# Performance work log

Hardware: AMD Instinct MI355X
Metric: run time of the kernel (lower is better)

Reference implementation:

```python
import jax, jax.numpy as jnp
import numpy as np

N = 65536          # total nodes (64 graphs x 1024 nodes)
E = 1048576        # total edges (avg degree 16)
F_IN, F_HID, F_OUT = 128, 128, 64


def setup_inputs() -> dict:
    key = jax.random.key(0)
    k1, k2, k3, k4, k5, k6, k7, k8 = jax.random.split(key, 8)
    x = jax.random.normal(k1, (N, F_IN), dtype=jnp.float32)
    edge_index = jax.random.randint(k2, (2, E), 0, N, dtype=jnp.int32)
    edge_weight = jax.random.uniform(k3, (E,), dtype=jnp.float32)
    batch = jnp.repeat(jnp.arange(64, dtype=jnp.int32), N // 64)
    s1 = 1.0 / np.sqrt(F_IN)
    s2 = 1.0 / np.sqrt(F_HID)
    W1 = jax.random.uniform(k4, (F_IN, F_HID), jnp.float32, -s1, s1)
    b1 = jnp.zeros((F_HID,), jnp.float32)
    W2 = jax.random.uniform(k5, (F_HID, F_HID), jnp.float32, -s2, s2)
    b2 = jnp.zeros((F_HID,), jnp.float32)
    fcW = jax.random.uniform(k6, (F_HID, F_OUT), jnp.float32, -s2, s2)
    fcb = jax.random.uniform(k7, (F_OUT,), jnp.float32, -s2, s2)
    return {"x": x, "edge_index": edge_index, "edge_weight": edge_weight,
            "batch": batch, "W1": W1, "b1": b1, "W2": W2, "b2": b2,
            "fcW": fcW, "fcb": fcb}


def gcn_conv(x, W, b, src, dst, ew, n_nodes):
    # PyG GCNConv: add self-loops (weight 1), symmetric normalization
    # deg[i] = 1 + sum of incoming edge weights at i
    deg = jax.ops.segment_sum(ew, dst, num_segments=n_nodes) + 1.0
    dinv = jax.lax.rsqrt(deg)                       # deg >= 1, no inf
    h = x @ W                                       # [N, F_out]
    norm = dinv[src] * ew * dinv[dst]               # [E]
    agg = jax.ops.segment_sum(h[src] * norm[:, None], dst, num_segments=n_nodes)
    agg = agg + h * (dinv * dinv)[:, None]          # self-loop term (1/deg)
    return agg + b


def reference(x, edge_index, edge_weight, batch, W1, b1, W2, b2, fcW, fcb):
    src, dst = edge_index[0], edge_index[1]
    n = x.shape[0]
    h = jax.nn.relu(gcn_conv(x, W1, b1, src, dst, edge_weight, n))
    h = jax.nn.relu(gcn_conv(h, W2, b2, src, dst, edge_weight, n))
    out = h @ fcW + fcb
    batch_size = int(batch.max()) + 1
    num_nodes = n // batch_size
    return out.reshape(batch_size, num_nodes, -1)
```

## Files before the change

### kernel.cpp

```cpp
#include <hip/hip_runtime.h>
#include <hip/hip_fp16.h>

#define N_NODES 65536
#define N_EDGES 1048576
#define F 128
#define NBUCK 256
#define BCAP 8192

typedef unsigned long long ull;
typedef _Float16 half8 __attribute__((ext_vector_type(8)));
typedef float floatx4 __attribute__((ext_vector_type(4)));


__global__ __launch_bounds__(256) void k_bpart(const int* __restrict__ srcArr,
                                               const int* __restrict__ dstArr,
                                               const float* __restrict__ ew,
                                               int* __restrict__ gfill,
                                               ull* __restrict__ brec) {
    __shared__ int hist[NBUCK];
    __shared__ int cur[NBUCK];
    int t = threadIdx.x;
    hist[t] = 0;
    __syncthreads();
    int base = blockIdx.x * 4096;
    int dv[16];
#pragma unroll
    for (int i = 0; i < 16; ++i) {
        dv[i] = dstArr[base + i * 256 + t];
        atomicAdd(&hist[dv[i] >> 8], 1);
    }
    __syncthreads();
    cur[t] = t * BCAP + atomicAdd(&gfill[t], hist[t]);
    __syncthreads();
#pragma unroll
    for (int i = 0; i < 16; ++i) {
        int e = base + i * 256 + t;
        int d = dv[i];
        unsigned int s = (unsigned int)srcArr[e];
        unsigned int wb = __float_as_uint(ew[e]);
        int pos = atomicAdd(&cur[d >> 8], 1);
        brec[pos] = ((ull)wb << 32) | ((ull)(d & 255) << 16) | (ull)s;
    }
}


__global__ __launch_bounds__(256) void k_build(const ull* __restrict__ brec,
                                               const int* __restrict__ gfill,
                                               float* __restrict__ dinv,
                                               ull* __restrict__ row_info,
                                               ull* __restrict__ edge8) {
    __shared__ ull packed[256];
    __shared__ int sc[256];
    __shared__ int cur[256];
    int t = threadIdx.x;
    int b = blockIdx.x;
    int cnt = gfill[b];
    int beg0 = b * BCAP;
    packed[t] = 0ULL;
    __syncthreads();

    for (int j = t; j < cnt; j += 256) {
        ull r = brec[beg0 + j];
        int dloc = (int)((r >> 16) & 255);
        float w = __uint_as_float((unsigned int)(r >> 32));
        ull fx = (ull)(w * 1073741824.0f);
        atomicAdd(&packed[dloc], (1ULL << 40) | fx);
    }
    __syncthreads();

    ull p = packed[t];
    int c = (int)(p >> 40);
    float deg = 1.0f + (float)(p & ((1ULL << 40) - 1)) * (1.0f / 1073741824.0f);
    dinv[b * 256 + t] = rsqrtf(deg);

    sc[t] = c;
    __syncthreads();
    for (int off = 1; off < 256; off <<= 1) {
        int tv = (t >= off) ? sc[t - off] : 0;
        __syncthreads();
        sc[t] += tv;
        __syncthreads();
    }
    int excl = sc[t] - c;
    row_info[b * 256 + t] = ((ull)(beg0 + excl) << 16) | (ull)c;
    cur[t] = beg0 + excl;
    __syncthreads();

    for (int j = t; j < cnt; j += 256) {
        ull r = brec[beg0 + j];
        int dloc = (int)((r >> 16) & 255);
        int pos = atomicAdd(&cur[dloc], 1);
        edge8[pos] = (r & 0xFFFFFFFF00000000ULL) | (r & 0xFFFFULL);
    }
}


__global__ __launch_bounds__(256) void k_gemm_mfma(const float* __restrict__ X,
                                                   const float* __restrict__ W,
                                                   const float* __restrict__ dinv,
                                                   __half* __restrict__ Y) {
    __shared__ _Float16 Ah[128][40];
    __shared__ _Float16 Al[128][40];
    __shared__ _Float16 Bh[128][40];
    __shared__ _Float16 Bl[128][40];

    const int tid = threadIdx.x;
    const int wv = tid >> 6;
    const int ln = tid & 63;
    const long rowbase = (long)blockIdx.x * 128;

    floatx4 acc[2][8];
#pragma unroll
    for (int i = 0; i < 2; ++i)
#pragma unroll
        for (int j = 0; j < 8; ++j) acc[i][j] = (floatx4)(0.f);

    for (int k0 = 0; k0 < 128; k0 += 32) {
        {
            int row = tid >> 1;
            int kh = (tid & 1) * 16;
            const float* src = &X[(rowbase + row) * 128 + k0 + kh];
            _Float16 hi[16], lo[16];
#pragma unroll
            for (int i = 0; i < 16; i += 4) {
                float4 v = *(const float4*)&src[i];
                hi[i + 0] = (_Float16)v.x; lo[i + 0] = (_Float16)(v.x - (float)hi[i + 0]);
                hi[i + 1] = (_Float16)v.y; lo[i + 1] = (_Float16)(v.y - (float)hi[i + 1]);
                hi[i + 2] = (_Float16)v.z; lo[i + 2] = (_Float16)(v.z - (float)hi[i + 2]);
                hi[i + 3] = (_Float16)v.w; lo[i + 3] = (_Float16)(v.w - (float)hi[i + 3]);
            }
            *(half8*)&Ah[row][kh] = *(half8*)&hi[0];
            *(half8*)&Ah[row][kh + 8] = *(half8*)&hi[8];
            *(half8*)&Al[row][kh] = *(half8*)&lo[0];
            *(half8*)&Al[row][kh + 8] = *(half8*)&lo[8];
        }
        {
            int n = tid & 127;
            int kh = (tid >> 7) * 16;
            _Float16 hi[16], lo[16];
#pragma unroll
            for (int i = 0; i < 16; ++i) {
                float v = W[(k0 + kh + i) * 128 + n];
                hi[i] = (_Float16)v;
                lo[i] = (_Float16)(v - (float)hi[i]);
            }
            *(half8*)&Bh[n][kh] = *(half8*)&hi[0];
            *(half8*)&Bh[n][kh + 8] = *(half8*)&hi[8];
            *(half8*)&Bl[n][kh] = *(half8*)&lo[0];
            *(half8*)&Bl[n][kh + 8] = *(half8*)&lo[8];
        }
        __syncthreads();

        int arow0 = wv * 32 + (ln & 15);
        int kq = (ln >> 4) * 8;
        half8 a_hi0 = *(const half8*)&Ah[arow0][kq];
        half8 a_hi1 = *(const half8*)&Ah[arow0 + 16][kq];
        half8 a_lo0 = *(const half8*)&Al[arow0][kq];
        half8 a_lo1 = *(const half8*)&Al[arow0 + 16][kq];
#pragma unroll
        for (int ct = 0; ct < 8; ++ct) {
            int bcol = ct * 16 + (ln & 15);
            half8 b_hi = *(const half8*)&Bh[bcol][kq];
            half8 b_lo = *(const half8*)&Bl[bcol][kq];
            acc[0][ct] = __builtin_amdgcn_mfma_f32_16x16x32_f16(a_hi0, b_hi, acc[0][ct], 0, 0, 0);
            acc[0][ct] = __builtin_amdgcn_mfma_f32_16x16x32_f16(a_hi0, b_lo, acc[0][ct], 0, 0, 0);
            acc[0][ct] = __builtin_amdgcn_mfma_f32_16x16x32_f16(a_lo0, b_hi, acc[0][ct], 0, 0, 0);
            acc[1][ct] = __builtin_amdgcn_mfma_f32_16x16x32_f16(a_hi1, b_hi, acc[1][ct], 0, 0, 0);
            acc[1][ct] = __builtin_amdgcn_mfma_f32_16x16x32_f16(a_hi1, b_lo, acc[1][ct], 0, 0, 0);
            acc[1][ct] = __builtin_amdgcn_mfma_f32_16x16x32_f16(a_lo1, b_hi, acc[1][ct], 0, 0, 0);
        }
        __syncthreads();
    }

#pragma unroll
    for (int rt = 0; rt < 2; ++rt)
#pragma unroll
        for (int reg = 0; reg < 4; ++reg) {
            long row = rowbase + wv * 32 + rt * 16 + (ln >> 4) * 4 + reg;
            float dv = dinv[row];
#pragma unroll
            for (int ct = 0; ct < 8; ++ct)
                Y[row * 128 + ct * 16 + (ln & 15)] = __float2half(acc[rt][ct][reg] * dv);
        }
}


__global__ __launch_bounds__(256) void k_gemm_mfma_h(const __half* __restrict__ X,
                                                     const float* __restrict__ W,
                                                     const float* __restrict__ dinv,
                                                     __half* __restrict__ Y) {
    __shared__ _Float16 Ah[128][40];
    __shared__ _Float16 Bh[128][40];
    __shared__ _Float16 Bl[128][40];

    const int tid = threadIdx.x;
    const int wv = tid >> 6;
    const int ln = tid & 63;
    const long rowbase = (long)blockIdx.x * 128;

    floatx4 acc[2][8];
#pragma unroll
    for (int i = 0; i < 2; ++i)
#pragma unroll
        for (int j = 0; j < 8; ++j) acc[i][j] = (floatx4)(0.f);

    for (int k0 = 0; k0 < 128; k0 += 32) {
        {
            int row = tid >> 1;
            int kh = (tid & 1) * 16;
            const __half* src = &X[(rowbase + row) * 128 + k0 + kh];
            *(half8*)&Ah[row][kh] = *(const half8*)&src[0];
            *(half8*)&Ah[row][kh + 8] = *(const half8*)&src[8];
        }
        {
            int n = tid & 127;
            int kh = (tid >> 7) * 16;
            _Float16 hi[16], lo[16];
#pragma unroll
            for (int i = 0; i < 16; ++i) {
                float v = W[(k0 + kh + i) * 128 + n];
                hi[i] = (_Float16)v;
                lo[i] = (_Float16)(v - (float)hi[i]);
            }
            *(half8*)&Bh[n][kh] = *(half8*)&hi[0];
            *(half8*)&Bh[n][kh + 8] = *(half8*)&hi[8];
            *(half8*)&Bl[n][kh] = *(half8*)&lo[0];
            *(half8*)&Bl[n][kh + 8] = *(half8*)&lo[8];
        }
        __syncthreads();

        int arow0 = wv * 32 + (ln & 15);
        int kq = (ln >> 4) * 8;
        half8 a0 = *(const half8*)&Ah[arow0][kq];
        half8 a1 = *(const half8*)&Ah[arow0 + 16][kq];
#pragma unroll
        for (int ct = 0; ct < 8; ++ct) {
            int bcol = ct * 16 + (ln & 15);
            half8 b_hi = *(const half8*)&Bh[bcol][kq];
            half8 b_lo = *(const half8*)&Bl[bcol][kq];
            acc[0][ct] = __builtin_amdgcn_mfma_f32_16x16x32_f16(a0, b_hi, acc[0][ct], 0, 0, 0);
            acc[0][ct] = __builtin_amdgcn_mfma_f32_16x16x32_f16(a0, b_lo, acc[0][ct], 0, 0, 0);
            acc[1][ct] = __builtin_amdgcn_mfma_f32_16x16x32_f16(a1, b_hi, acc[1][ct], 0, 0, 0);
            acc[1][ct] = __builtin_amdgcn_mfma_f32_16x16x32_f16(a1, b_lo, acc[1][ct], 0, 0, 0);
        }
        __syncthreads();
    }

#pragma unroll
    for (int rt = 0; rt < 2; ++rt)
#pragma unroll
        for (int reg = 0; reg < 4; ++reg) {
            long row = rowbase + wv * 32 + rt * 16 + (ln >> 4) * 4 + reg;
            float dv = dinv[row];
#pragma unroll
            for (int ct = 0; ct < 8; ++ct)
                Y[row * 128 + ct * 16 + (ln & 15)] = __float2half(acc[rt][ct][reg] * dv);
        }
}


__global__ __launch_bounds__(256) void k_fc_mfma_h(const __half* __restrict__ X,
                                                   const float* __restrict__ W,
                                                   const float* __restrict__ bias,
                                                   float* __restrict__ Y) {
    __shared__ _Float16 Ah[128][40];
    __shared__ _Float16 Bh[64][40];
    __shared__ _Float16 Bl[64][40];

    const int tid = threadIdx.x;
    const int wv = tid >> 6;
    const int ln = tid & 63;
    const long rowbase = (long)blockIdx.x * 128;

    floatx4 acc[2][4];
#pragma unroll
    for (int i = 0; i < 2; ++i)
#pragma unroll
        for (int j = 0; j < 4; ++j) acc[i][j] = (floatx4)(0.f);

    for (int k0 = 0; k0 < 128; k0 += 32) {
        {
            int row = tid >> 1;
            int kh = (tid & 1) * 16;
            const __half* src = &X[(rowbase + row) * 128 + k0 + kh];
            *(half8*)&Ah[row][kh] = *(const half8*)&src[0];
            *(half8*)&Ah[row][kh + 8] = *(const half8*)&src[8];
        }
        {
            int n = tid & 63;
            int kh = (tid >> 6) * 8;
            _Float16 hi[8], lo[8];
#pragma unroll
            for (int i = 0; i < 8; ++i) {
                float v = W[(k0 + kh + i) * 64 + n];
                hi[i] = (_Float16)v;
                lo[i] = (_Float16)(v - (float)hi[i]);
            }
            *(half8*)&Bh[n][kh] = *(half8*)&hi[0];
            *(half8*)&Bl[n][kh] = *(half8*)&lo[0];
        }
        __syncthreads();

        int arow0 = wv * 32 + (ln & 15);
        int kq = (ln >> 4) * 8;
        half8 a0 = *(const half8*)&Ah[arow0][kq];
        half8 a1 = *(const half8*)&Ah[arow0 + 16][kq];
#pragma unroll
        for (int ct = 0; ct < 4; ++ct) {
            int bcol = ct * 16 + (ln & 15);
            half8 b_hi = *(const half8*)&Bh[bcol][kq];
            half8 b_lo = *(const half8*)&Bl[bcol][kq];
            acc[0][ct] = __builtin_amdgcn_mfma_f32_16x16x32_f16(a0, b_hi, acc[0][ct], 0, 0, 0);
            acc[0][ct] = __builtin_amdgcn_mfma_f32_16x16x32_f16(a0, b_lo, acc[0][ct], 0, 0, 0);
            acc[1][ct] = __builtin_amdgcn_mfma_f32_16x16x32_f16(a1, b_hi, acc[1][ct], 0, 0, 0);
            acc[1][ct] = __builtin_amdgcn_mfma_f32_16x16x32_f16(a1, b_lo, acc[1][ct], 0, 0, 0);
        }
        __syncthreads();
    }

#pragma unroll
    for (int rt = 0; rt < 2; ++rt)
#pragma unroll
        for (int ct = 0; ct < 4; ++ct)
#pragma unroll
            for (int reg = 0; reg < 4; ++reg) {
                long row = rowbase + wv * 32 + rt * 16 + (ln >> 4) * 4 + reg;
                int col = ct * 16 + (ln & 15);
                Y[row * 64 + col] = acc[rt][ct][reg] + bias[col];
            }
}


__global__ __launch_bounds__(256) void k_aggregate(const __half2* __restrict__ hlin,
                                                   const ull* __restrict__ row_info,
                                                   const ull* __restrict__ edge8,
                                                   const float* __restrict__ dinv,
                                                   const float* __restrict__ bias,
                                                   __half2* __restrict__ out) {
    int wave = threadIdx.x >> 6;
    int lane = threadIdx.x & 63;
    int n = (blockIdx.x << 2) + wave;

    float di = dinv[n];
    ull info = row_info[n];
    int beg = (int)(info >> 16);
    int end = beg + (int)(info & 0xFFFF);

    float2 h0 = __half22float2(hlin[(size_t)n * 64 + lane]);
    float2 a0, a1, a2, a3, a4, a5, a6, a7;
    a0 = a1 = a2 = a3 = a4 = a5 = a6 = a7 = make_float2(0.f, 0.f);

    for (int jb = beg; jb < end; jb += 64) {
        int nload = end - jb;
        if (nload > 64) nload = 64;
        ull r = 0ULL;
        if (lane < nload) r = __builtin_nontemporal_load(&edge8[jb + lane]);
        for (int q = 0; q < nload; q += 8) {
            ull r0 = __shfl(r, q + 0), r1 = __shfl(r, q + 1);
            ull r2 = __shfl(r, q + 2), r3 = __shfl(r, q + 3);
            ull r4 = __shfl(r, q + 4), r5 = __shfl(r, q + 5);
            ull r6 = __shfl(r, q + 6), r7 = __shfl(r, q + 7);
            int s0 = (int)(r0 & 0xFFFF), s1 = (int)(r1 & 0xFFFF);
            int s2 = (int)(r2 & 0xFFFF), s3 = (int)(r3 & 0xFFFF);
            int s4 = (int)(r4 & 0xFFFF), s5 = (int)(r5 & 0xFFFF);
            int s6 = (int)(r6 & 0xFFFF), s7 = (int)(r7 & 0xFFFF);
            float c0 = __uint_as_float((unsigned int)(r0 >> 32));
            float c1 = __uint_as_float((unsigned int)(r1 >> 32));
            float c2 = __uint_as_float((unsigned int)(r2 >> 32));
            float c3 = __uint_as_float((unsigned int)(r3 >> 32));
            float c4 = __uint_as_float((unsigned int)(r4 >> 32));
            float c5 = __uint_as_float((unsigned int)(r5 >> 32));
            float c6 = __uint_as_float((unsigned int)(r6 >> 32));
            float c7 = __uint_as_float((unsigned int)(r7 >> 32));
            __half2 g0 = hlin[(size_t)s0 * 64 + lane];
            __half2 g1 = hlin[(size_t)s1 * 64 + lane];
            __half2 g2 = hlin[(size_t)s2 * 64 + lane];
            __half2 g3 = hlin[(size_t)s3 * 64 + lane];
            __half2 g4 = hlin[(size_t)s4 * 64 + lane];
            __half2 g5 = hlin[(size_t)s5 * 64 + lane];
            __half2 g6 = hlin[(size_t)s6 * 64 + lane];
            __half2 g7 = hlin[(size_t)s7 * 64 + lane];
            float2 f0 = __half22float2(g0), f1 = __half22float2(g1);
            float2 f2 = __half22float2(g2), f3 = __half22float2(g3);
            float2 f4 = __half22float2(g4), f5 = __half22float2(g5);
            float2 f6 = __half22float2(g6), f7 = __half22float2(g7);
            a0.x = fmaf(c0, f0.x, a0.x); a0.y = fmaf(c0, f0.y, a0.y);
            a1.x = fmaf(c1, f1.x, a1.x); a1.y = fmaf(c1, f1.y, a1.y);
            a2.x = fmaf(c2, f2.x, a2.x); a2.y = fmaf(c2, f2.y, a2.y);
            a3.x = fmaf(c3, f3.x, a3.x); a3.y = fmaf(c3, f3.y, a3.y);
            a4.x = fmaf(c4, f4.x, a4.x); a4.y = fmaf(c4, f4.y, a4.y);
            a5.x = fmaf(c5, f5.x, a5.x); a5.y = fmaf(c5, f5.y, a5.y);
            a6.x = fmaf(c6, f6.x, a6.x); a6.y = fmaf(c6, f6.y, a6.y);
            a7.x = fmaf(c7, f7.x, a7.x); a7.y = fmaf(c7, f7.y, a7.y);
        }
    }

    float2 sum;
    sum.x = ((a0.x + a1.x) + (a2.x + a3.x)) + ((a4.x + a5.x) + (a6.x + a7.x));
    sum.y = ((a0.y + a1.y) + (a2.y + a3.y)) + ((a4.y + a5.y) + (a6.y + a7.y));

    float2 bb = ((const float2*)bias)[lane];
    float ox = fmaxf(fmaf(di, sum.x + h0.x, bb.x), 0.f);
    float oy = fmaxf(fmaf(di, sum.y + h0.y, bb.y), 0.f);
    out[(size_t)n * 64 + lane] = __floats2half2_rn(ox, oy);
}


extern "C" void kernel_launch(void* const* d_in, const int* in_sizes, int n_in,
                              void* d_out, int out_size, void* d_ws, size_t ws_size,
                              hipStream_t stream) {
    const float* x   = (const float*)d_in[0];
    const int*   ei  = (const int*)d_in[1];
    const float* ew  = (const float*)d_in[2];
    const float* W1  = (const float*)d_in[4];
    const float* b1  = (const float*)d_in[5];
    const float* W2  = (const float*)d_in[6];
    const float* b2  = (const float*)d_in[7];
    const float* fcW = (const float*)d_in[8];
    const float* fcb = (const float*)d_in[9];
    float* out = (float*)d_out;

    const int* srcArr = ei;
    const int* dstArr = ei + N_EDGES;

    char* w = (char*)d_ws;
    int* gfill = (int*)w;              w += 256 * 4;
    float* dinv = (float*)w;           w += (size_t)N_NODES * 4;
    ull* row_info = (ull*)w;           w += (size_t)N_NODES * 8;
    ull* edge8 = (ull*)w;              w += (size_t)NBUCK * BCAP * 8;
    __half* bufH = (__half*)w;         w += (size_t)N_NODES * F * 2;
    __half* bufB = (__half*)w;         w += (size_t)N_NODES * F * 2;
    ull* brec = (ull*)bufH;

    hipMemsetAsync(gfill, 0, 256 * 4, stream);
    k_bpart<<<N_EDGES / 4096, 256, 0, stream>>>(srcArr, dstArr, ew, gfill, brec);
    k_build<<<NBUCK, 256, 0, stream>>>(brec, gfill, dinv, row_info, edge8);

    k_gemm_mfma<<<512, 256, 0, stream>>>(x, W1, dinv, bufH);
    k_aggregate<<<N_NODES / 4, 256, 0, stream>>>((const __half2*)bufH, row_info, edge8,
                                                 dinv, b1, (__half2*)bufB);
    k_gemm_mfma_h<<<512, 256, 0, stream>>>(bufB, W2, dinv, bufH);
    k_aggregate<<<N_NODES / 4, 256, 0, stream>>>((const __half2*)bufH, row_info, edge8,
                                                 dinv, b2, (__half2*)bufB);
    k_fc_mfma_h<<<512, 256, 0, stream>>>(bufB, fcW, fcb, out);
}
```

Measured before the change: 153.8 us.

## Fuse second-layer aggregation with final FC projection and replace memset with kernel

The second aggregation kernel now also does the final linear layer. Each block stages the full 128x64 fp32 fcW matrix in shared memory, each wave writes its node's ReLU activations to LDS, and the wave then computes the 64 outputs with scalar FMAs. This removes the separate MFMA FC kernel and the fp16 intermediate round trip through global memory. In exchange, every one of the 16384 blocks reloads 32 KB of weights and holds about 34 KB of LDS, which may cut occupancy for the latency-bound gather. The hipMemsetAsync on the bucket counters is also replaced by a tiny zeroing kernel.

```diff
diff --git a/kernel.cpp b/kernel.cpp
--- a/kernel.cpp
+++ b/kernel.cpp
@@ -10,6 +10,11 @@
 typedef unsigned long long ull;
 typedef _Float16 half8 __attribute__((ext_vector_type(8)));
 typedef float floatx4 __attribute__((ext_vector_type(4)));
+
+
+__global__ __launch_bounds__(256) void k_zero256(int* gfill) {
+    gfill[threadIdx.x] = 0;
+}
 
 
 __global__ __launch_bounds__(256) void k_bpart(const int* __restrict__ srcArr,
@@ -256,78 +261,6 @@
             for (int ct = 0; ct < 8; ++ct)
                 Y[row * 128 + ct * 16 + (ln & 15)] = __float2half(acc[rt][ct][reg] * dv);
         }
-}
-
-
-__global__ __launch_bounds__(256) void k_fc_mfma_h(const __half* __restrict__ X,
-                                                   const float* __restrict__ W,
-                                                   const float* __restrict__ bias,
-                                                   float* __restrict__ Y) {
-    __shared__ _Float16 Ah[128][40];
-    __shared__ _Float16 Bh[64][40];
-    __shared__ _Float16 Bl[64][40];
-
-    const int tid = threadIdx.x;
-    const int wv = tid >> 6;
-    const int ln = tid & 63;
-    const long rowbase = (long)blockIdx.x * 128;
-
-    floatx4 acc[2][4];
-#pragma unroll
-    for (int i = 0; i < 2; ++i)
-#pragma unroll
-        for (int j = 0; j < 4; ++j) acc[i][j] = (floatx4)(0.f);
-
-    for (int k0 = 0; k0 < 128; k0 += 32) {
-        {
-            int row = tid >> 1;
-            int kh = (tid & 1) * 16;
-            const __half* src = &X[(rowbase + row) * 128 + k0 + kh];
-            *(half8*)&Ah[row][kh] = *(const half8*)&src[0];
-            *(half8*)&Ah[row][kh + 8] = *(const half8*)&src[8];
-        }
-        {
-            int n = tid & 63;
-            int kh = (tid >> 6) * 8;
-            _Float16 hi[8], lo[8];
-#pragma unroll
-            for (int i = 0; i < 8; ++i) {
-                float v = W[(k0 + kh + i) * 64 + n];
-                hi[i] = (_Float16)v;
-                lo[i] = (_Float16)(v - (float)hi[i]);
-            }
-            *(half8*)&Bh[n][kh] = *(half8*)&hi[0];
-            *(half8*)&Bl[n][kh] = *(half8*)&lo[0];
-        }
-        __syncthreads();
-
-        int arow0 = wv * 32 + (ln & 15);
-        int kq = (ln >> 4) * 8;
-        half8 a0 = *(const half8*)&Ah[arow0][kq];
-        half8 a1 = *(const half8*)&Ah[arow0 + 16][kq];
-#pragma unroll
-        for (int ct = 0; ct < 4; ++ct) {
-            int bcol = ct * 16 + (ln & 15);
-            half8 b_hi = *(const half8*)&Bh[bcol][kq];
-            half8 b_lo = *(const half8*)&Bl[bcol][kq];
-            acc[0][ct] = __builtin_amdgcn_mfma_f32_16x16x32_f16(a0, b_hi, acc[0][ct], 0, 0, 0);
-            acc[0][ct] = __builtin_amdgcn_mfma_f32_16x16x32_f16(a0, b_lo, acc[0][ct], 0, 0, 0);
-            acc[1][ct] = __builtin_amdgcn_mfma_f32_16x16x32_f16(a1, b_hi, acc[1][ct], 0, 0, 0);
-            acc[1][ct] = __builtin_amdgcn_mfma_f32_16x16x32_f16(a1, b_lo, acc[1][ct], 0, 0, 0);
-        }
-        __syncthreads();
-    }
-
-#pragma unroll
-    for (int rt = 0; rt < 2; ++rt)
-#pragma unroll
-        for (int ct = 0; ct < 4; ++ct)
-#pragma unroll
-            for (int reg = 0; reg < 4; ++reg) {
-                long row = rowbase + wv * 32 + rt * 16 + (ln >> 4) * 4 + reg;
-                int col = ct * 16 + (ln & 15);
-                Y[row * 64 + col] = acc[rt][ct][reg] + bias[col];
-            }
 }
 
 
@@ -406,6 +339,104 @@
 }
 
 
+__global__ __launch_bounds__(256) void k_aggregate_fc(const __half2* __restrict__ hlin,
+                                                      const ull* __restrict__ row_info,
+                                                      const ull* __restrict__ edge8,
+                                                      const float* __restrict__ dinv,
+                                                      const float* __restrict__ bias,
+                                                      const float* __restrict__ fcW,
+                                                      const float* __restrict__ fcb,
+                                                      float* __restrict__ outF) {
+    __shared__ float Ws[128 * 64];
+    __shared__ float acts[4][128];
+
+    int tid = threadIdx.x;
+    int wave = tid >> 6;
+    int lane = tid & 63;
+    int n = (blockIdx.x << 2) + wave;
+
+    {
+        const float4* src = (const float4*)fcW;
+        float4* dst = (float4*)Ws;
+        for (int i = tid; i < 2048; i += 256) dst[i] = src[i];
+    }
+    __syncthreads();
+
+    float di = dinv[n];
+    ull info = row_info[n];
+    int beg = (int)(info >> 16);
+    int end = beg + (int)(info & 0xFFFF);
+
+    float2 h0 = __half22float2(hlin[(size_t)n * 64 + lane]);
+    float2 a0, a1, a2, a3, a4, a5, a6, a7;
+    a0 = a1 = a2 = a3 = a4 = a5 = a6 = a7 = make_float2(0.f, 0.f);
+
+    for (int jb = beg; jb < end; jb += 64) {
+        int nload = end - jb;
+        if (nload > 64) nload = 64;
+        ull r = 0ULL;
+        if (lane < nload) r = __builtin_nontemporal_load(&edge8[jb + lane]);
+        for (int q = 0; q < nload; q += 8) {
+            ull r0 = __shfl(r, q + 0), r1 = __shfl(r, q + 1);
+            ull r2 = __shfl(r, q + 2), r3 = __shfl(r, q + 3);
+            ull r4 = __shfl(r, q + 4), r5 = __shfl(r, q + 5);
+            ull r6 = __shfl(r, q + 6), r7 = __shfl(r, q + 7);
+            int s0 = (int)(r0 & 0xFFFF), s1 = (int)(r1 & 0xFFFF);
+            int s2 = (int)(r2 & 0xFFFF), s3 = (int)(r3 & 0xFFFF);
+            int s4 = (int)(r4 & 0xFFFF), s5 = (int)(r5 & 0xFFFF);
+            int s6 = (int)(r6 & 0xFFFF), s7 = (int)(r7 & 0xFFFF);
+            float c0 = __uint_as_float((unsigned int)(r0 >> 32));
+            float c1 = __uint_as_float((unsigned int)(r1 >> 32));
+            float c2 = __uint_as_float((unsigned int)(r2 >> 32));
+            float c3 = __uint_as_float((unsigned int)(r3 >> 32));
+            float c4 = __uint_as_float((unsigned int)(r4 >> 32));
+            float c5 = __uint_as_float((unsigned int)(r5 >> 32));
+            float c6 = __uint_as_float((unsigned int)(r6 >> 32));
+            float c7 = __uint_as_float((unsigned int)(r7 >> 32));
+            __half2 g0 = hlin[(size_t)s0 * 64 + lane];
+            __half2 g1 = hlin[(size_t)s1 * 64 + lane];
+            __half2 g2 = hlin[(size_t)s2 * 64 + lane];
+            __half2 g3 = hlin[(size_t)s3 * 64 + lane];
+            __half2 g4 = hlin[(size_t)s4 * 64 + lane];
+            __half2 g5 = hlin[(size_t)s5 * 64 + lane];
+            __half2 g6 = hlin[(size_t)s6 * 64 + lane];
+            __half2 g7 = hlin[(size_t)s7 * 64 + lane];
+            float2 f0 = __half22float2(g0), f1 = __half22float2(g1);
+            float2 f2 = __half22float2(g2), f3 = __half22float2(g3);
+            float2 f4 = __half22float2(g4), f5 = __half22float2(g5);
+            float2 f6 = __half22float2(g6), f7 = __half22float2(g7);
+            a0.x = fmaf(c0, f0.x, a0.x); a0.y = fmaf(c0, f0.y, a0.y);
+            a1.x = fmaf(c1, f1.x, a1.x); a1.y = fmaf(c1, f1.y, a1.y);
+            a2.x = fmaf(c2, f2.x, a2.x); a2.y = fmaf(c2, f2.y, a2.y);
+            a3.x = fmaf(c3, f3.x, a3.x); a3.y = fmaf(c3, f3.y, a3.y);
+            a4.x = fmaf(c4, f4.x, a4.x); a4.y = fmaf(c4, f4.y, a4.y);
+            a5.x = fmaf(c5, f5.x, a5.x); a5.y = fmaf(c5, f5.y, a5.y);
+            a6.x = fmaf(c6, f6.x, a6.x); a6.y = fmaf(c6, f6.y, a6.y);
+            a7.x = fmaf(c7, f7.x, a7.x); a7.y = fmaf(c7, f7.y, a7.y);
+        }
+    }
+
+    float2 sum;
+    sum.x = ((a0.x + a1.x) + (a2.x + a3.x)) + ((a4.x + a5.x) + (a6.x + a7.x));
+    sum.y = ((a0.y + a1.y) + (a2.y + a3.y)) + ((a4.y + a5.y) + (a6.y + a7.y));
+
+    float2 bb = ((const float2*)bias)[lane];
+    float ox = fmaxf(fmaf(di, sum.x + h0.x, bb.x), 0.f);
+    float oy = fmaxf(fmaf(di, sum.y + h0.y, bb.y), 0.f);
+
+    acts[wave][lane * 2]     = ox;
+    acts[wave][lane * 2 + 1] = oy;
+    __builtin_amdgcn_wave_barrier();
+
+    float o = fcb[lane];
+    const float* arow = acts[wave];
+#pragma unroll 8
+    for (int k = 0; k < 128; ++k)
+        o = fmaf(arow[k], Ws[k * 64 + lane], o);
+    outF[(size_t)n * 64 + lane] = o;
+}
+
+
 extern "C" void kernel_launch(void* const* d_in, const int* in_sizes, int n_in,
                               void* d_out, int out_size, void* d_ws, size_t ws_size,
                               hipStream_t stream) {
@@ -432,7 +463,7 @@
     __half* bufB = (__half*)w;         w += (size_t)N_NODES * F * 2;
     ull* brec = (ull*)bufH;
 
-    hipMemsetAsync(gfill, 0, 256 * 4, stream);
+    k_zero256<<<1, 256, 0, stream>>>(gfill);
     k_bpart<<<N_EDGES / 4096, 256, 0, stream>>>(srcArr, dstArr, ew, gfill, brec);
     k_build<<<NBUCK, 256, 0, stream>>>(brec, gfill, dinv, row_info, edge8);
 
@@ -440,7 +471,6 @@
     k_aggregate<<<N_NODES / 4, 256, 0, stream>>>((const __half2*)bufH, row_info, edge8,
                                                  dinv, b1, (__half2*)bufB);
     k_gemm_mfma_h<<<512, 256, 0, stream>>>(bufB, W2, dinv, bufH);
-    k_aggregate<<<N_NODES / 4, 256, 0, stream>>>((const __half2*)bufH, row_info, edge8,
-                                                 dinv, b2, (__half2*)bufB);
-    k_fc_mfma_h<<<512, 256, 0, stream>>>(bufB, fcW, fcb, out);
-}
+    k_aggregate_fc<<<N_NODES / 4, 256, 0, stream>>>((const __half2*)bufH, row_info,
+                                                    edge8, dinv, b2, fcW, fcb, out);
+}
```

After: 210.2 us. 1.37x slower.
